# Optimization experiments

Hardware: AMD Instinct MI355X
Metric: run time of the kernel (lower is better)

The kernel has to match this reference:

```python
import jax, jax.numpy as jnp
import numpy as np

L, N, D = 2, 100000, 128
TRACE_HID, MVC_DIM, MVC_HID = 256, 128, 64
NUM_EDGE = 1600000
TAU = 0.5


def setup_inputs() -> dict:
    key = jax.random.key(0)
    ks = jax.random.split(key, 9)
    trace_all = jax.random.normal(ks[0], (L, N, D), dtype=jnp.float32)
    W_lin = jax.random.normal(ks[1], (TRACE_HID, L * D), dtype=jnp.float32) * 0.05
    W_lin2 = jax.random.normal(ks[2], (MVC_DIM, TRACE_HID), dtype=jnp.float32) * 0.05
    W_fc1 = jax.random.normal(ks[3], (MVC_HID, 2 * MVC_DIM), dtype=jnp.float32) * 0.05
    b_fc1 = jax.random.normal(ks[4], (MVC_HID,), dtype=jnp.float32) * 0.05
    W_fc2 = jax.random.normal(ks[5], (2, MVC_HID), dtype=jnp.float32) * 0.05
    b_fc2 = jax.random.normal(ks[6], (2,), dtype=jnp.float32) * 0.05
    u = jax.random.uniform(ks[7], (NUM_EDGE, 2), dtype=jnp.float32, minval=1e-6, maxval=1.0 - 1e-6)
    gumbel = -jnp.log(-jnp.log(u))  # standard Gumbel(0,1) noise
    edge_index = jax.random.randint(ks[8], (2, 3 * NUM_EDGE), 0, N, dtype=jnp.int32)
    return {
        "trace_all": trace_all, "W_lin": W_lin, "W_lin2": W_lin2,
        "W_fc1": W_fc1, "b_fc1": b_fc1, "W_fc2": W_fc2, "b_fc2": b_fc2,
        "gumbel": gumbel, "edge_index": edge_index, "num_edge": NUM_EDGE,
    }


def reference(trace_all, W_lin, W_lin2, W_fc1, b_fc1, W_fc2, b_fc2, gumbel, edge_index, num_edge):
    # --- TraceMLP: [L, N, d] -> mvc [N, mvc_dim] (eval mode: dropout is identity)
    l, n, d = trace_all.shape
    x = jnp.transpose(trace_all, (1, 0, 2)).reshape(n, l * d)      # [N, L*d]
    h = jax.nn.relu(x @ W_lin.T)                                   # [N, trace_hidden]
    mvc = h @ W_lin2.T                                             # [N, mvc_dim]
    norm = jnp.maximum(jnp.linalg.norm(mvc, axis=1, keepdims=True), 1e-12)
    mvc = mvc / norm                                               # F.normalize(p=2, dim=1)

    # --- EdgeScoringNet over non-slow edges (first num_edge columns)
    src = edge_index[0, :num_edge]
    dst = edge_index[1, :num_edge]
    comb = jnp.concatenate([mvc[src], mvc[dst]], axis=1)           # [E, 2*mvc_dim]
    h2 = jax.nn.relu(comb @ W_fc1.T + b_fc1)                       # [E, mvc_hidden]
    scores = h2 @ W_fc2.T + b_fc2                                  # [E, 2]

    # --- gumbel_softmax(tau=0.5, hard=True)[:, 0] (straight-through)
    y_soft = jax.nn.softmax((scores + gumbel) / TAU, axis=-1)
    y_hard = jax.nn.one_hot(jnp.argmax(y_soft, axis=-1), 2, dtype=y_soft.dtype)
    ret = y_hard - jax.lax.stop_gradient(y_soft) + y_soft
    active = ret[:, 0]                                             # [E], values in {0,1}

    # --- train_mask: first block = active, next two blocks = 1 - active
    train_mask = jnp.concatenate([active, 1.0 - active, 1.0 - active])  # [3*E]
    return train_mask
```

## Files before the change

### kernel.cpp

```cpp
#include <hip/hip_runtime.h>

#define NN   100000
#define EE   1600000
#define EROW 4800000

typedef _Float16 half8 __attribute__((ext_vector_type(8)));
typedef _Float16 half4 __attribute__((ext_vector_type(4)));
typedef float    f32x4 __attribute__((ext_vector_type(4)));

__device__ __forceinline__ float4 ld4(const float* p){ return *(const float4*)p; }

__device__ __forceinline__ unsigned splitf(float v) {
    _Float16 h = (_Float16)v;
    float r = v - (float)h;
    _Float16 l = (_Float16)(r * 2048.0f);
    union { _Float16 f; unsigned short u; } uh, ul;
    uh.f = h; ul.f = l;
    return (unsigned)uh.u | ((unsigned)ul.u << 16);
}

__device__ __forceinline__ void dma16(const void* g, void* l) {
    __builtin_amdgcn_global_load_lds(
        (const __attribute__((address_space(1))) unsigned*)((size_t)g),
        (__attribute__((address_space(3))) unsigned*)((size_t)l),
        16, 0, 0);
}

__global__ __launch_bounds__(256)
void prep_w(const float* __restrict__ W1, const float* __restrict__ W2,
            const float* __restrict__ W3, unsigned* __restrict__ o1,
            unsigned* __restrict__ o2, unsigned* __restrict__ o3)
{
    int idx = blockIdx.x * 256 + threadIdx.x;
    if (idx < 65536) {
        o1[idx] = splitf(W1[idx]);
    } else if (idx < 98304) {
        int i = idx - 65536;
        o2[i] = splitf(W2[i]);
    } else {
        int i = idx - 98304;
        int j = i >> 7, k = i & 127;
        o3[i] = splitf(W3[(j & 63) * 256 + (j >> 6) * 128 + k]);
    }
}

template<int SRCA, int EPI, int K>
__global__ __launch_bounds__(256, 2)
void gemm_mfma(const void* __restrict__ Asrc, const unsigned* __restrict__ Bw,
               const float* __restrict__ bias, unsigned* __restrict__ outS,
               float* __restrict__ outF, unsigned short* __restrict__ outH,
               int M, int No)
{
    __shared__ __align__(16) unsigned bufA[2][128 * 32];
    __shared__ __align__(16) unsigned bufB[2][128 * 32];
    __shared__ float sqv[128][2];

    const int t     = threadIdx.x;
    const int w     = t >> 6;
    const int wm    = w >> 1;
    const int wn    = w & 1;
    const int lane  = t & 63;
    const int lm    = lane & 15;
    const int q     = lane >> 4;
    const int mBase = blockIdx.x * 128;
    const int nBase = blockIdx.y * 128;

    const int col16 = (lane & 7) ^ (lane >> 3);

    f32x4 aH[4][4], aM[4][4];
#pragma unroll
    for (int i = 0; i < 4; ++i)
#pragma unroll
        for (int j = 0; j < 4; ++j) {
            aH[i][j] = (f32x4){0.f, 0.f, 0.f, 0.f};
            aM[i][j] = (f32x4){0.f, 0.f, 0.f, 0.f};
        }

    auto stage = [&](int sb, int kt) {
#pragma unroll
        for (int c = 0; c < 4; ++c) {
            const int row = w * 32 + c * 8 + (lane >> 3);
            unsigned* ldsA = &bufA[sb][w * 1024 + c * 256];
            unsigned* ldsB = &bufB[sb][w * 1024 + c * 256];
            int rgA = mBase + row; rgA = rgA < M ? rgA : M - 1;
            if (SRCA == 0) {
                const int kg    = kt * 32;
                const int plane = kg >> 7;
                const int ktl   = kg & 127;
                const float* gA = (const float*)Asrc
                    + (size_t)plane * ((size_t)NN * 128)
                    + (size_t)rgA * 128 + ktl + col16 * 4;
                dma16(gA, ldsA);
            } else {
                const unsigned* gA = (const unsigned*)Asrc
                    + (size_t)rgA * K + kt * 32 + col16 * 4;
                dma16(gA, ldsA);
            }
            const unsigned* gB = Bw + (size_t)(nBase + row) * K + kt * 32 + col16 * 4;
            dma16(gB, ldsB);
        }
    };

    union HL { uint4 u; half8 h; };

    constexpr int NK = K / 32;
    stage(0, 0);
    __syncthreads();

#pragma unroll 2
    for (int kt = 0; kt < NK; ++kt) {
        const int b = kt & 1;
        if (kt + 1 < NK) stage(b ^ 1, kt + 1);

        half8 fAh[4], fAl[4], fBh[4], fBl[4];

#pragma unroll
        for (int i = 0; i < 4; ++i) {
            const int r = wm * 64 + i * 16 + lm;
            const int x = r & 7;
            const unsigned* p0p = &bufA[b][r * 32 + (((2 * q) ^ x) << 2)];
            const unsigned* p1p = &bufA[b][r * 32 + ((((2 * q) | 1) ^ x) << 2)];
            HL H, L;
            if (SRCA == 0) {
                float4 f0 = *(const float4*)p0p;
                float4 f1 = *(const float4*)p1p;
                unsigned p0 = splitf(f0.x), p1 = splitf(f0.y);
                unsigned p2 = splitf(f0.z), p3 = splitf(f0.w);
                unsigned p4 = splitf(f1.x), p5 = splitf(f1.y);
                unsigned p6 = splitf(f1.z), p7 = splitf(f1.w);
                H.u.x = (p0 & 0xffffu) | (p1 << 16);
                H.u.y = (p2 & 0xffffu) | (p3 << 16);
                H.u.z = (p4 & 0xffffu) | (p5 << 16);
                H.u.w = (p6 & 0xffffu) | (p7 << 16);
                L.u.x = (p0 >> 16) | (p1 & 0xffff0000u);
                L.u.y = (p2 >> 16) | (p3 & 0xffff0000u);
                L.u.z = (p4 >> 16) | (p5 & 0xffff0000u);
                L.u.w = (p6 >> 16) | (p7 & 0xffff0000u);
            } else {
                uint4 u0 = *(const uint4*)p0p;
                uint4 u1 = *(const uint4*)p1p;
                H.u.x = (u0.x & 0xffffu) | (u0.y << 16);
                H.u.y = (u0.z & 0xffffu) | (u0.w << 16);
                H.u.z = (u1.x & 0xffffu) | (u1.y << 16);
                H.u.w = (u1.z & 0xffffu) | (u1.w << 16);
                L.u.x = (u0.x >> 16) | (u0.y & 0xffff0000u);
                L.u.y = (u0.z >> 16) | (u0.w & 0xffff0000u);
                L.u.z = (u1.x >> 16) | (u1.y & 0xffff0000u);
                L.u.w = (u1.z >> 16) | (u1.w & 0xffff0000u);
            }
            fAh[i] = H.h;
            fAl[i] = L.h;
        }

#pragma unroll
        for (int j = 0; j < 4; ++j) {
            const int r = wn * 64 + j * 16 + lm;
            const int x = r & 7;
            uint4 u0 = *(const uint4*)&bufB[b][r * 32 + (((2 * q) ^ x) << 2)];
            uint4 u1 = *(const uint4*)&bufB[b][r * 32 + ((((2 * q) | 1) ^ x) << 2)];
            HL H, L;
            H.u.x = (u0.x & 0xffffu) | (u0.y << 16);
            H.u.y = (u0.z & 0xffffu) | (u0.w << 16);
            H.u.z = (u1.x & 0xffffu) | (u1.y << 16);
            H.u.w = (u1.z & 0xffffu) | (u1.w << 16);
            L.u.x = (u0.x >> 16) | (u0.y & 0xffff0000u);
            L.u.y = (u0.z >> 16) | (u0.w & 0xffff0000u);
            L.u.z = (u1.x >> 16) | (u1.y & 0xffff0000u);
            L.u.w = (u1.z >> 16) | (u1.w & 0xffff0000u);
            fBh[j] = H.h;
            fBl[j] = L.h;
        }

        __builtin_amdgcn_s_setprio(1);
#pragma unroll
        for (int i = 0; i < 4; ++i)
#pragma unroll
            for (int j = 0; j < 4; ++j)
                aH[i][j] = __builtin_amdgcn_mfma_f32_16x16x32_f16(fAh[i], fBh[j], aH[i][j], 0, 0, 0);
#pragma unroll
        for (int i = 0; i < 4; ++i)
#pragma unroll
            for (int j = 0; j < 4; ++j)
                aM[i][j] = __builtin_amdgcn_mfma_f32_16x16x32_f16(fAh[i], fBl[j], aM[i][j], 0, 0, 0);
#pragma unroll
        for (int i = 0; i < 4; ++i)
#pragma unroll
            for (int j = 0; j < 4; ++j)
                aM[i][j] = __builtin_amdgcn_mfma_f32_16x16x32_f16(fAl[i], fBh[j], aM[i][j], 0, 0, 0);
        __builtin_amdgcn_s_setprio(0);

        if (kt + 1 < NK) __syncthreads();
    }

    const float cM = 1.0f / 2048.0f;
#pragma unroll
    for (int i = 0; i < 4; ++i)
#pragma unroll
        for (int j = 0; j < 4; ++j)
            aH[i][j] = aH[i][j] + aM[i][j] * cM;

    float nm[4][4];
    if (EPI == 1) {
#pragma unroll
        for (int i = 0; i < 4; ++i)
#pragma unroll
            for (int r = 0; r < 4; ++r) {
                float s = 0.f;
#pragma unroll
                for (int j = 0; j < 4; ++j) { float x = aH[i][j][r]; s = fmaf(x, x, s); }
#pragma unroll
                for (int off = 1; off < 16; off <<= 1) s += __shfl_xor(s, off, 16);
                if (lm == 0) sqv[wm * 64 + i * 16 + q * 4 + r][wn] = s;
            }
        __syncthreads();
#pragma unroll
        for (int i = 0; i < 4; ++i)
#pragma unroll
            for (int r = 0; r < 4; ++r) {
                const int rl = wm * 64 + i * 16 + q * 4 + r;
                nm[i][r] = fmaxf(sqrtf(sqv[rl][0] + sqv[rl][1]), 1e-12f);
            }
    }

    float bj[4] = {0.f, 0.f, 0.f, 0.f};
    if (EPI == 2 && wn == 0) {
#pragma unroll
        for (int j = 0; j < 4; ++j) bj[j] = bias[j * 16 + lm];
    }

#pragma unroll
    for (int i = 0; i < 4; ++i)
#pragma unroll
        for (int r = 0; r < 4; ++r) {
            const int m = mBase + wm * 64 + i * 16 + q * 4 + r;
            if (m < M) {
#pragma unroll
                for (int j = 0; j < 4; ++j) {
                    const int c = nBase + wn * 64 + j * 16 + lm;
                    float v = aH[i][j][r];
                    if (EPI == 0) { v = fmaxf(v, 0.f); outS[(size_t)m * No + c] = splitf(v); }
                    if (EPI == 1) { v = v / nm[i][r];  outS[(size_t)m * No + c] = splitf(v); }
                    if (EPI == 2) {
                        v += bj[j];
                        outF[(size_t)m * No + c] = v;
                        union { _Float16 f; unsigned short u; } cv; cv.f = (_Float16)v;
                        outH[(size_t)m * No + c] = cv.u;
                    }
                }
            }
        }
}

#define EPB 128
__global__ __launch_bounds__(256, 4)
void edge_k(const unsigned short* __restrict__ pH, const float* __restrict__ p,
            const int* __restrict__ ei, const float* __restrict__ gum,
            const float* __restrict__ W2, const float* __restrict__ b2,
            float* __restrict__ out)
{
    __shared__ int   sidx[EPB];
    __shared__ int   didx[EPB];
    __shared__ float gl[2 * EPB];
    __shared__ float act[EPB];

    const int t  = threadIdx.x;
    const int e0 = blockIdx.x * EPB;

    if (t < EPB) sidx[t] = ei[e0 + t];
    else         didx[t - EPB] = ei[EROW + e0 + (t - EPB)];
    gl[t] = gum[(size_t)e0 * 2 + t];
    __syncthreads();

    const int j   = t & 15;
    const int grp = t >> 4;
    const float4 w0 = ld4(&W2[j * 4]);
    const float4 w1 = ld4(&W2[64 + j * 4]);
    const float4 dk = make_float4(w0.x - w1.x, w0.y - w1.y,
                                  w0.z - w1.z, w0.w - w1.w);
    const float4 dw = make_float4(fabsf(dk.x), fabsf(dk.y),
                                  fabsf(dk.z), fabsf(dk.w));
    const float b20 = b2[0], b21 = b2[1];
    const float dB  = b20 - b21;

    union U8 { uint2 u; half4 h; };
    U8 ua[8], ub[8];
#pragma unroll
    for (int it = 0; it < 8; ++it) {
        const int el = grp * 8 + it;
        ua[it].u = *(const uint2*)&pH[(size_t)sidx[el] * 128 + j * 4];
        ub[it].u = *(const uint2*)&pH[(size_t)didx[el] * 128 + 64 + j * 4];
    }

#pragma unroll
    for (int it = 0; it < 8; ++it) {
        const int el = grp * 8 + it;
        const float a0 = (float)ua[it].h[0], a1 = (float)ua[it].h[1];
        const float a2 = (float)ua[it].h[2], a3 = (float)ua[it].h[3];
        const float c0 = (float)ub[it].h[0], c1 = (float)ub[it].h[1];
        const float c2 = (float)ub[it].h[2], c3 = (float)ub[it].h[3];
        const float r0 = fmaxf(a0 + c0, 0.f);
        const float r1 = fmaxf(a1 + c1, 0.f);
        const float r2 = fmaxf(a2 + c2, 0.f);
        const float r3 = fmaxf(a3 + c3, 0.f);
        float sc = r0 * dk.x + r1 * dk.y + r2 * dk.z + r3 * dk.w;
        float eb = dw.x * (fabsf(a0) + fabsf(c0)) + dw.y * (fabsf(a1) + fabsf(c1))
                 + dw.z * (fabsf(a2) + fabsf(c2)) + dw.w * (fabsf(a3) + fabsf(c3));
#pragma unroll
        for (int off = 1; off < 16; off <<= 1) {
            sc += __shfl_xor(sc, off, 16);
            eb += __shfl_xor(eb, off, 16);
        }
        const float g0 = gl[el * 2], g1 = gl[el * 2 + 1];
        const float gap = sc + dB + (g0 - g1);
        const float bound = eb * 0.0009765625f + 2e-5f;
        float av;
        if (fabsf(gap) > bound) {
            av = (gap >= 0.f) ? 1.f : 0.f;
        } else {
            const float4 pa = ld4(&p[(size_t)sidx[el] * 128 + j * 4]);
            const float4 pb = ld4(&p[(size_t)didx[el] * 128 + 64 + j * 4]);
            const float q0 = fmaxf(pa.x + pb.x, 0.f);
            const float q1 = fmaxf(pa.y + pb.y, 0.f);
            const float q2 = fmaxf(pa.z + pb.z, 0.f);
            const float q3 = fmaxf(pa.w + pb.w, 0.f);
            float t0 = q0 * w0.x + q1 * w0.y + q2 * w0.z + q3 * w0.w;
            float t1 = q0 * w1.x + q1 * w1.y + q2 * w1.z + q3 * w1.w;
#pragma unroll
            for (int off = 1; off < 16; off <<= 1) {
                t0 += __shfl_xor(t0, off, 16);
                t1 += __shfl_xor(t1, off, 16);
            }
            const float ge = (t0 + b20 + g0) - (t1 + b21 + g1);
            av = (ge >= 0.f) ? 1.f : 0.f;
        }
        if (j == 0) act[el] = av;
    }
    __syncthreads();

    if (t < EPB) {
        const float a = act[t];
        const size_t e = (size_t)e0 + t;
        out[e]                  = a;
        out[EE + e]             = 1.f - a;
        out[2 * (size_t)EE + e] = 1.f - a;
    }
}

extern "C" void kernel_launch(void* const* d_in, const int* in_sizes, int n_in,
                              void* d_out, int out_size, void* d_ws, size_t ws_size,
                              hipStream_t stream)
{
    const float* trace  = (const float*)d_in[0];
    const float* W_lin  = (const float*)d_in[1];
    const float* W_lin2 = (const float*)d_in[2];
    const float* W_fc1  = (const float*)d_in[3];
    const float* b_fc1  = (const float*)d_in[4];
    const float* W_fc2  = (const float*)d_in[5];
    const float* b_fc2  = (const float*)d_in[6];
    const float* gum    = (const float*)d_in[7];
    const int*   ei     = (const int*)  d_in[8];
    float*       out    = (float*)d_out;

    char* ws = (char*)d_ws;
    unsigned*       hpl = (unsigned*)ws;
    unsigned*       mpl = (unsigned*)(ws + (size_t)NN * 256 * 4);
    unsigned*       W1i = (unsigned*)(ws + (size_t)NN * 256 * 4 + (size_t)NN * 128 * 4);
    unsigned*       W2i = W1i + 65536;
    unsigned*       W3i = W2i + 32768;
    float*          p   = (float*)ws;
    unsigned short* pH  = (unsigned short*)(ws + (size_t)NN * 128 * 4);

    prep_w<<<448, 256, 0, stream>>>(W_lin, W_lin2, W_fc1, W1i, W2i, W3i);

    const int mB = (NN + 127) / 128;

    gemm_mfma<0, 0, 256><<<dim3(mB, 2), 256, 0, stream>>>(trace, W1i, nullptr, hpl, nullptr, nullptr, NN, 256);
    gemm_mfma<1, 1, 256><<<dim3(mB, 1), 256, 0, stream>>>(hpl, W2i, nullptr, mpl, nullptr, nullptr, NN, 128);
    gemm_mfma<1, 2, 128><<<dim3(mB, 1), 256, 0, stream>>>(mpl, W3i, b_fc1, nullptr, p, pH, NN, 128);
    edge_k<<<EE / EPB, 256, 0, stream>>>(pH, p, ei, gum, W_fc2, b_fc2, out);
}
```

Before: 369.9 us.

## Shrink GEMM tile to 128x64 and defer L2 normalization into the third GEMM

The MFMA GEMM tile drops from 128x128 to 128x64 with all four waves split along M. Each kernel launches twice as many blocks, and the launch bound rises to 3 blocks per CU for higher occupancy. The row L2 normalization moves out of the second GEMM's epilogue. The third GEMM now computes the row sum of squares from its A-operand fragments and divides its outputs by the norm, which is valid because normalization is a row scale that commutes with the linear layer. The cost is more redundant A-tile loads across N blocks and extra ALU work per fragment in the third GEMM.

```diff
diff --git a/kernel.cpp b/kernel.cpp
--- a/kernel.cpp
+++ b/kernel.cpp
@@ -45,57 +45,59 @@
 }
 
 template<int SRCA, int EPI, int K>
-__global__ __launch_bounds__(256, 2)
+__global__ __launch_bounds__(256, 3)
 void gemm_mfma(const void* __restrict__ Asrc, const unsigned* __restrict__ Bw,
                const float* __restrict__ bias, unsigned* __restrict__ outS,
                float* __restrict__ outF, unsigned short* __restrict__ outH,
                int M, int No)
 {
     __shared__ __align__(16) unsigned bufA[2][128 * 32];
-    __shared__ __align__(16) unsigned bufB[2][128 * 32];
-    __shared__ float sqv[128][2];
+    __shared__ __align__(16) unsigned bufB[2][64 * 32];
+    __shared__ float sqv[128];
 
     const int t     = threadIdx.x;
     const int w     = t >> 6;
-    const int wm    = w >> 1;
-    const int wn    = w & 1;
     const int lane  = t & 63;
     const int lm    = lane & 15;
     const int q     = lane >> 4;
     const int mBase = blockIdx.x * 128;
-    const int nBase = blockIdx.y * 128;
+    const int nBase = blockIdx.y * 64;
 
     const int col16 = (lane & 7) ^ (lane >> 3);
 
-    f32x4 aH[4][4], aM[4][4];
-#pragma unroll
-    for (int i = 0; i < 4; ++i)
+    f32x4 aH[2][4], aM[2][4];
+#pragma unroll
+    for (int i = 0; i < 2; ++i)
 #pragma unroll
         for (int j = 0; j < 4; ++j) {
             aH[i][j] = (f32x4){0.f, 0.f, 0.f, 0.f};
             aM[i][j] = (f32x4){0.f, 0.f, 0.f, 0.f};
         }
 
+    float ssq[2] = {0.f, 0.f};
+
     auto stage = [&](int sb, int kt) {
 #pragma unroll
         for (int c = 0; c < 4; ++c) {
             const int row = w * 32 + c * 8 + (lane >> 3);
             unsigned* ldsA = &bufA[sb][w * 1024 + c * 256];
-            unsigned* ldsB = &bufB[sb][w * 1024 + c * 256];
             int rgA = mBase + row; rgA = rgA < M ? rgA : M - 1;
             if (SRCA == 0) {
-                const int kg    = kt * 32;
-                const int plane = kg >> 7;
-                const int ktl   = kg & 127;
+                const int kg = kt * 32;
                 const float* gA = (const float*)Asrc
-                    + (size_t)plane * ((size_t)NN * 128)
-                    + (size_t)rgA * 128 + ktl + col16 * 4;
+                    + (size_t)(kg >> 7) * ((size_t)NN * 128)
+                    + (size_t)rgA * 128 + (kg & 127) + col16 * 4;
                 dma16(gA, ldsA);
             } else {
                 const unsigned* gA = (const unsigned*)Asrc
                     + (size_t)rgA * K + kt * 32 + col16 * 4;
                 dma16(gA, ldsA);
             }
+        }
+#pragma unroll
+        for (int c = 0; c < 2; ++c) {
+            const int row = w * 16 + c * 8 + (lane >> 3);
+            unsigned* ldsB = &bufB[sb][w * 512 + c * 256];
             const unsigned* gB = Bw + (size_t)(nBase + row) * K + kt * 32 + col16 * 4;
             dma16(gB, ldsB);
         }
@@ -112,12 +114,11 @@
         const int b = kt & 1;
         if (kt + 1 < NK) stage(b ^ 1, kt + 1);
 
-        half8 fAh[4], fAl[4], fBh[4], fBl[4];
-
-#pragma unroll
-        for (int i = 0; i < 4; ++i) {
-            const int r = wm * 64 + i * 16 + lm;
-            const int x = r & 7;
+        half8 fAh[2], fAl[2];
+#pragma unroll
+        for (int i = 0; i < 2; ++i) {
+            const int r = w * 32 + i * 16 + lm;
+            const int x = lm & 7;
             const unsigned* p0p = &bufA[b][r * 32 + (((2 * q) ^ x) << 2)];
             const unsigned* p1p = &bufA[b][r * 32 + ((((2 * q) | 1) ^ x) << 2)];
             HL H, L;
@@ -150,14 +151,22 @@
             }
             fAh[i] = H.h;
             fAl[i] = L.h;
-        }
-
+            if (EPI == 2) {
+#pragma unroll
+                for (int e = 0; e < 8; ++e) {
+                    float v = (float)fAh[i][e] + (float)fAl[i][e] * (1.0f / 2048.0f);
+                    ssq[i] = fmaf(v, v, ssq[i]);
+                }
+            }
+        }
+
+        __builtin_amdgcn_s_setprio(1);
 #pragma unroll
         for (int j = 0; j < 4; ++j) {
-            const int r = wn * 64 + j * 16 + lm;
-            const int x = r & 7;
-            uint4 u0 = *(const uint4*)&bufB[b][r * 32 + (((2 * q) ^ x) << 2)];
-            uint4 u1 = *(const uint4*)&bufB[b][r * 32 + ((((2 * q) | 1) ^ x) << 2)];
+            const int rB = j * 16 + lm;
+            const int x = lm & 7;
+            uint4 u0 = *(const uint4*)&bufB[b][rB * 32 + (((2 * q) ^ x) << 2)];
+            uint4 u1 = *(const uint4*)&bufB[b][rB * 32 + ((((2 * q) | 1) ^ x) << 2)];
             HL H, L;
             H.u.x = (u0.x & 0xffffu) | (u0.y << 16);
             H.u.y = (u0.z & 0xffffu) | (u0.w << 16);
@@ -167,26 +176,13 @@
             L.u.y = (u0.z >> 16) | (u0.w & 0xffff0000u);
             L.u.z = (u1.x >> 16) | (u1.y & 0xffff0000u);
             L.u.w = (u1.z >> 16) | (u1.w & 0xffff0000u);
-            fBh[j] = H.h;
-            fBl[j] = L.h;
-        }
-
-        __builtin_amdgcn_s_setprio(1);
-#pragma unroll
-        for (int i = 0; i < 4; ++i)
-#pragma unroll
-            for (int j = 0; j < 4; ++j)
-                aH[i][j] = __builtin_amdgcn_mfma_f32_16x16x32_f16(fAh[i], fBh[j], aH[i][j], 0, 0, 0);
-#pragma unroll
-        for (int i = 0; i < 4; ++i)
-#pragma unroll
-            for (int j = 0; j < 4; ++j)
-                aM[i][j] = __builtin_amdgcn_mfma_f32_16x16x32_f16(fAh[i], fBl[j], aM[i][j], 0, 0, 0);
-#pragma unroll
-        for (int i = 0; i < 4; ++i)
-#pragma unroll
-            for (int j = 0; j < 4; ++j)
-                aM[i][j] = __builtin_amdgcn_mfma_f32_16x16x32_f16(fAl[i], fBh[j], aM[i][j], 0, 0, 0);
+#pragma unroll
+            for (int i = 0; i < 2; ++i) {
+                aH[i][j] = __builtin_amdgcn_mfma_f32_16x16x32_f16(fAh[i], H.h, aH[i][j], 0, 0, 0);
+                aM[i][j] = __builtin_amdgcn_mfma_f32_16x16x32_f16(fAh[i], L.h, aM[i][j], 0, 0, 0);
+                aM[i][j] = __builtin_amdgcn_mfma_f32_16x16x32_f16(fAl[i], H.h, aM[i][j], 0, 0, 0);
+            }
+        }
         __builtin_amdgcn_s_setprio(0);
 
         if (kt + 1 < NK) __syncthreads();
@@ -194,54 +190,45 @@
 
     const float cM = 1.0f / 2048.0f;
 #pragma unroll
-    for (int i = 0; i < 4; ++i)
+    for (int i = 0; i < 2; ++i)
 #pragma unroll
         for (int j = 0; j < 4; ++j)
             aH[i][j] = aH[i][j] + aM[i][j] * cM;
 
-    float nm[4][4];
-    if (EPI == 1) {
-#pragma unroll
-        for (int i = 0; i < 4; ++i)
-#pragma unroll
-            for (int r = 0; r < 4; ++r) {
-                float s = 0.f;
-#pragma unroll
-                for (int j = 0; j < 4; ++j) { float x = aH[i][j][r]; s = fmaf(x, x, s); }
-#pragma unroll
-                for (int off = 1; off < 16; off <<= 1) s += __shfl_xor(s, off, 16);
-                if (lm == 0) sqv[wm * 64 + i * 16 + q * 4 + r][wn] = s;
-            }
+    if (EPI == 2) {
+#pragma unroll
+        for (int i = 0; i < 2; ++i) {
+            float s = ssq[i];
+            s += __shfl_xor(s, 16);
+            s += __shfl_xor(s, 32);
+            if (q == 0) sqv[w * 32 + i * 16 + lm] = s;
+        }
         __syncthreads();
-#pragma unroll
-        for (int i = 0; i < 4; ++i)
-#pragma unroll
-            for (int r = 0; r < 4; ++r) {
-                const int rl = wm * 64 + i * 16 + q * 4 + r;
-                nm[i][r] = fmaxf(sqrtf(sqv[rl][0] + sqv[rl][1]), 1e-12f);
-            }
     }
 
     float bj[4] = {0.f, 0.f, 0.f, 0.f};
-    if (EPI == 2 && wn == 0) {
+    if (EPI == 2 && nBase == 0 && bias) {
 #pragma unroll
         for (int j = 0; j < 4; ++j) bj[j] = bias[j * 16 + lm];
     }
 
 #pragma unroll
-    for (int i = 0; i < 4; ++i)
+    for (int i = 0; i < 2; ++i)
 #pragma unroll
         for (int r = 0; r < 4; ++r) {
-            const int m = mBase + wm * 64 + i * 16 + q * 4 + r;
+            const int m = mBase + w * 32 + i * 16 + q * 4 + r;
             if (m < M) {
+                float nm = 1.f;
+                if (EPI == 2)
+                    nm = fmaxf(sqrtf(sqv[w * 32 + i * 16 + q * 4 + r]), 1e-12f);
 #pragma unroll
                 for (int j = 0; j < 4; ++j) {
-                    const int c = nBase + wn * 64 + j * 16 + lm;
+                    const int c = nBase + j * 16 + lm;
                     float v = aH[i][j][r];
                     if (EPI == 0) { v = fmaxf(v, 0.f); outS[(size_t)m * No + c] = splitf(v); }
-                    if (EPI == 1) { v = v / nm[i][r];  outS[(size_t)m * No + c] = splitf(v); }
+                    if (EPI == 1) { outS[(size_t)m * No + c] = splitf(v); }
                     if (EPI == 2) {
-                        v += bj[j];
+                        v = v / nm + bj[j];
                         outF[(size_t)m * No + c] = v;
                         union { _Float16 f; unsigned short u; } cv; cv.f = (_Float16)v;
                         outH[(size_t)m * No + c] = cv.u;
@@ -374,8 +361,8 @@
 
     const int mB = (NN + 127) / 128;
 
-    gemm_mfma<0, 0, 256><<<dim3(mB, 2), 256, 0, stream>>>(trace, W1i, nullptr, hpl, nullptr, nullptr, NN, 256);
-    gemm_mfma<1, 1, 256><<<dim3(mB, 1), 256, 0, stream>>>(hpl, W2i, nullptr, mpl, nullptr, nullptr, NN, 128);
-    gemm_mfma<1, 2, 128><<<dim3(mB, 1), 256, 0, stream>>>(mpl, W3i, b_fc1, nullptr, p, pH, NN, 128);
+    gemm_mfma<0, 0, 256><<<dim3(mB, 4), 256, 0, stream>>>(trace, W1i, nullptr, hpl, nullptr, nullptr, NN, 256);
+    gemm_mfma<1, 1, 256><<<dim3(mB, 2), 256, 0, stream>>>(hpl, W2i, nullptr, mpl, nullptr, nullptr, NN, 128);
+    gemm_mfma<1, 2, 128><<<dim3(mB, 2), 256, 0, stream>>>(mpl, W3i, b_fc1, nullptr, p, pH, NN, 128);
     edge_k<<<EE / EPB, 256, 0, stream>>>(pH, p, ei, gum, W_fc2, b_fc2, out);
 }
```

Result: slower. 390.8 us (+5.6%).

## Fuse second and third GEMMs and store projection as fp16 hi/lo halves

Applied to the files above, without the earlier changes.

Merges the normalize GEMM and the fc1 projection GEMM into one kernel. The normalized mvc tile stays in LDS as split-fp16 pairs and is immediately multiplied by W_fc1, which removes the mvc round trip through global memory and one launch. The fp32 projection buffer is replaced by a separate fp16 low-residual array. The edge kernel's fallback path rebuilds near-fp32 values from the high halves it already loaded plus the low halves. The cost is reading W3 fragments directly from global memory inside the fused kernel, plus extra LDS pressure.

```diff
diff --git a/kernel.cpp b/kernel.cpp
--- a/kernel.cpp
+++ b/kernel.cpp
@@ -44,16 +44,13 @@
     }
 }
 
-template<int SRCA, int EPI, int K>
+template<int SRCA, int K>
 __global__ __launch_bounds__(256, 2)
 void gemm_mfma(const void* __restrict__ Asrc, const unsigned* __restrict__ Bw,
-               const float* __restrict__ bias, unsigned* __restrict__ outS,
-               float* __restrict__ outF, unsigned short* __restrict__ outH,
-               int M, int No)
+               unsigned* __restrict__ outS, int M, int No)
 {
     __shared__ __align__(16) unsigned bufA[2][128 * 32];
     __shared__ __align__(16) unsigned bufB[2][128 * 32];
-    __shared__ float sqv[128][2];
 
     const int t     = threadIdx.x;
     const int w     = t >> 6;
@@ -84,12 +81,10 @@
             unsigned* ldsB = &bufB[sb][w * 1024 + c * 256];
             int rgA = mBase + row; rgA = rgA < M ? rgA : M - 1;
             if (SRCA == 0) {
-                const int kg    = kt * 32;
-                const int plane = kg >> 7;
-                const int ktl   = kg & 127;
+                const int kg = kt * 32;
                 const float* gA = (const float*)Asrc
-                    + (size_t)plane * ((size_t)NN * 128)
-                    + (size_t)rgA * 128 + ktl + col16 * 4;
+                    + (size_t)(kg >> 7) * ((size_t)NN * 128)
+                    + (size_t)rgA * 128 + (kg & 127) + col16 * 4;
                 dma16(gA, ldsA);
             } else {
                 const unsigned* gA = (const unsigned*)Asrc
@@ -199,35 +194,6 @@
         for (int j = 0; j < 4; ++j)
             aH[i][j] = aH[i][j] + aM[i][j] * cM;
 
-    float nm[4][4];
-    if (EPI == 1) {
-#pragma unroll
-        for (int i = 0; i < 4; ++i)
-#pragma unroll
-            for (int r = 0; r < 4; ++r) {
-                float s = 0.f;
-#pragma unroll
-                for (int j = 0; j < 4; ++j) { float x = aH[i][j][r]; s = fmaf(x, x, s); }
-#pragma unroll
-                for (int off = 1; off < 16; off <<= 1) s += __shfl_xor(s, off, 16);
-                if (lm == 0) sqv[wm * 64 + i * 16 + q * 4 + r][wn] = s;
-            }
-        __syncthreads();
-#pragma unroll
-        for (int i = 0; i < 4; ++i)
-#pragma unroll
-            for (int r = 0; r < 4; ++r) {
-                const int rl = wm * 64 + i * 16 + q * 4 + r;
-                nm[i][r] = fmaxf(sqrtf(sqv[rl][0] + sqv[rl][1]), 1e-12f);
-            }
-    }
-
-    float bj[4] = {0.f, 0.f, 0.f, 0.f};
-    if (EPI == 2 && wn == 0) {
-#pragma unroll
-        for (int j = 0; j < 4; ++j) bj[j] = bias[j * 16 + lm];
-    }
-
 #pragma unroll
     for (int i = 0; i < 4; ++i)
 #pragma unroll
@@ -237,23 +203,237 @@
 #pragma unroll
                 for (int j = 0; j < 4; ++j) {
                     const int c = nBase + wn * 64 + j * 16 + lm;
-                    float v = aH[i][j][r];
-                    if (EPI == 0) { v = fmaxf(v, 0.f); outS[(size_t)m * No + c] = splitf(v); }
-                    if (EPI == 1) { v = v / nm[i][r];  outS[(size_t)m * No + c] = splitf(v); }
-                    if (EPI == 2) {
-                        v += bj[j];
-                        outF[(size_t)m * No + c] = v;
-                        union { _Float16 f; unsigned short u; } cv; cv.f = (_Float16)v;
-                        outH[(size_t)m * No + c] = cv.u;
-                    }
+                    float v = fmaxf(aH[i][j][r], 0.f);
+                    outS[(size_t)m * No + c] = splitf(v);
                 }
             }
         }
 }
 
+__global__ __launch_bounds__(256, 2)
+void gemm23(const unsigned* __restrict__ Apl, const unsigned* __restrict__ W2i,
+            const unsigned* __restrict__ W3i, const float* __restrict__ bias,
+            unsigned short* __restrict__ pHo, unsigned short* __restrict__ pLo,
+            int M)
+{
+    __shared__ __align__(16) unsigned smem[16384];
+    __shared__ float sqv[128][2];
+    unsigned (*bufA)[128 * 32] = (unsigned(*)[128 * 32])(smem);
+    unsigned (*bufB)[128 * 32] = (unsigned(*)[128 * 32])(smem + 8192);
+    unsigned* mld = smem;
+
+    const int t     = threadIdx.x;
+    const int w     = t >> 6;
+    const int wm    = w >> 1;
+    const int wn    = w & 1;
+    const int lane  = t & 63;
+    const int lm    = lane & 15;
+    const int q     = lane >> 4;
+    const int mBase = blockIdx.x * 128;
+
+    const int col16 = (lane & 7) ^ (lane >> 3);
+    const float cM = 1.0f / 2048.0f;
+
+    f32x4 aH[4][4], aM[4][4];
+#pragma unroll
+    for (int i = 0; i < 4; ++i)
+#pragma unroll
+        for (int j = 0; j < 4; ++j) {
+            aH[i][j] = (f32x4){0.f, 0.f, 0.f, 0.f};
+            aM[i][j] = (f32x4){0.f, 0.f, 0.f, 0.f};
+        }
+
+    auto stage = [&](int sb, int kt) {
+#pragma unroll
+        for (int c = 0; c < 4; ++c) {
+            const int row = w * 32 + c * 8 + (lane >> 3);
+            unsigned* ldsA = &bufA[sb][w * 1024 + c * 256];
+            unsigned* ldsB = &bufB[sb][w * 1024 + c * 256];
+            int rgA = mBase + row; rgA = rgA < M ? rgA : M - 1;
+            const unsigned* gA = Apl + (size_t)rgA * 256 + kt * 32 + col16 * 4;
+            dma16(gA, ldsA);
+            const unsigned* gB = W2i + (size_t)row * 256 + kt * 32 + col16 * 4;
+            dma16(gB, ldsB);
+        }
+    };
+
+    union HL { uint4 u; half8 h; };
+
+    auto deint = [&](uint4 u0, uint4 u1, half8& hh, half8& hl) {
+        HL H, L;
+        H.u.x = (u0.x & 0xffffu) | (u0.y << 16);
+        H.u.y = (u0.z & 0xffffu) | (u0.w << 16);
+        H.u.z = (u1.x & 0xffffu) | (u1.y << 16);
+        H.u.w = (u1.z & 0xffffu) | (u1.w << 16);
+        L.u.x = (u0.x >> 16) | (u0.y & 0xffff0000u);
+        L.u.y = (u0.z >> 16) | (u0.w & 0xffff0000u);
+        L.u.z = (u1.x >> 16) | (u1.y & 0xffff0000u);
+        L.u.w = (u1.z >> 16) | (u1.w & 0xffff0000u);
+        hh = H.h; hl = L.h;
+    };
+
+    stage(0, 0);
+    __syncthreads();
+
+#pragma unroll 2
+    for (int kt = 0; kt < 8; ++kt) {
+        const int b = kt & 1;
+        if (kt + 1 < 8) stage(b ^ 1, kt + 1);
+
+        half8 fAh[4], fAl[4], fBh[4], fBl[4];
+#pragma unroll
+        for (int i = 0; i < 4; ++i) {
+            const int r = wm * 64 + i * 16 + lm;
+            const int x = r & 7;
+            uint4 u0 = *(const uint4*)&bufA[b][r * 32 + (((2 * q) ^ x) << 2)];
+            uint4 u1 = *(const uint4*)&bufA[b][r * 32 + ((((2 * q) | 1) ^ x) << 2)];
+            deint(u0, u1, fAh[i], fAl[i]);
+        }
+#pragma unroll
+        for (int j = 0; j < 4; ++j) {
+            const int r = wn * 64 + j * 16 + lm;
+            const int x = r & 7;
+            uint4 u0 = *(const uint4*)&bufB[b][r * 32 + (((2 * q) ^ x) << 2)];
+            uint4 u1 = *(const uint4*)&bufB[b][r * 32 + ((((2 * q) | 1) ^ x) << 2)];
+            deint(u0, u1, fBh[j], fBl[j]);
+        }
+
+        __builtin_amdgcn_s_setprio(1);
+#pragma unroll
+        for (int i = 0; i < 4; ++i)
+#pragma unroll
+            for (int j = 0; j < 4; ++j)
+                aH[i][j] = __builtin_amdgcn_mfma_f32_16x16x32_f16(fAh[i], fBh[j], aH[i][j], 0, 0, 0);
+#pragma unroll
+        for (int i = 0; i < 4; ++i)
+#pragma unroll
+            for (int j = 0; j < 4; ++j)
+                aM[i][j] = __builtin_amdgcn_mfma_f32_16x16x32_f16(fAh[i], fBl[j], aM[i][j], 0, 0, 0);
+#pragma unroll
+        for (int i = 0; i < 4; ++i)
+#pragma unroll
+            for (int j = 0; j < 4; ++j)
+                aM[i][j] = __builtin_amdgcn_mfma_f32_16x16x32_f16(fAl[i], fBh[j], aM[i][j], 0, 0, 0);
+        __builtin_amdgcn_s_setprio(0);
+
+        if (kt + 1 < 8) __syncthreads();
+    }
+
+#pragma unroll
+    for (int i = 0; i < 4; ++i)
+#pragma unroll
+        for (int j = 0; j < 4; ++j)
+            aH[i][j] = aH[i][j] + aM[i][j] * cM;
+
+#pragma unroll
+    for (int i = 0; i < 4; ++i)
+#pragma unroll
+        for (int r = 0; r < 4; ++r) {
+            float s = 0.f;
+#pragma unroll
+            for (int j = 0; j < 4; ++j) { float x = aH[i][j][r]; s = fmaf(x, x, s); }
+#pragma unroll
+            for (int off = 1; off < 16; off <<= 1) s += __shfl_xor(s, off, 16);
+            if (lm == 0) sqv[wm * 64 + i * 16 + q * 4 + r][wn] = s;
+        }
+    __syncthreads();
+
+#pragma unroll
+    for (int i = 0; i < 4; ++i)
+#pragma unroll
+        for (int r = 0; r < 4; ++r) {
+            const int rl = wm * 64 + i * 16 + q * 4 + r;
+            const float nm = fmaxf(sqrtf(sqv[rl][0] + sqv[rl][1]), 1e-12f);
+#pragma unroll
+            for (int j = 0; j < 4; ++j) {
+                const int col = wn * 64 + j * 16 + lm;
+                const int ch  = (col >> 2) ^ (rl & 15);
+                mld[rl * 128 + (ch << 2) + (col & 3)] = splitf(aH[i][j][r] / nm);
+            }
+        }
+    __syncthreads();
+
+#pragma unroll
+    for (int i = 0; i < 4; ++i)
+#pragma unroll
+        for (int j = 0; j < 4; ++j) {
+            aH[i][j] = (f32x4){0.f, 0.f, 0.f, 0.f};
+            aM[i][j] = (f32x4){0.f, 0.f, 0.f, 0.f};
+        }
+
+#pragma unroll
+    for (int kt = 0; kt < 4; ++kt) {
+        half8 fAh[4], fAl[4], fBh[4], fBl[4];
+#pragma unroll
+        for (int i = 0; i < 4; ++i) {
+            const int row = wm * 64 + i * 16 + lm;
+            const int x = row & 15;
+            const int c0 = kt * 8 + 2 * q;
+            uint4 u0 = *(const uint4*)&mld[row * 128 + ((c0 ^ x) << 2)];
+            uint4 u1 = *(const uint4*)&mld[row * 128 + (((c0 + 1) ^ x) << 2)];
+            deint(u0, u1, fAh[i], fAl[i]);
+        }
+#pragma unroll
+        for (int j = 0; j < 4; ++j) {
+            const int row = wn * 64 + j * 16 + lm;
+            const unsigned* bp = W3i + (size_t)row * 128 + kt * 32 + q * 8;
+            uint4 u0 = *(const uint4*)bp;
+            uint4 u1 = *(const uint4*)(bp + 4);
+            deint(u0, u1, fBh[j], fBl[j]);
+        }
+
+        __builtin_amdgcn_s_setprio(1);
+#pragma unroll
+        for (int i = 0; i < 4; ++i)
+#pragma unroll
+            for (int j = 0; j < 4; ++j)
+                aH[i][j] = __builtin_amdgcn_mfma_f32_16x16x32_f16(fAh[i], fBh[j], aH[i][j], 0, 0, 0);
+#pragma unroll
+        for (int i = 0; i < 4; ++i)
+#pragma unroll
+            for (int j = 0; j < 4; ++j)
+                aM[i][j] = __builtin_amdgcn_mfma_f32_16x16x32_f16(fAh[i], fBl[j], aM[i][j], 0, 0, 0);
+#pragma unroll
+        for (int i = 0; i < 4; ++i)
+#pragma unroll
+            for (int j = 0; j < 4; ++j)
+                aM[i][j] = __builtin_amdgcn_mfma_f32_16x16x32_f16(fAl[i], fBh[j], aM[i][j], 0, 0, 0);
+        __builtin_amdgcn_s_setprio(0);
+    }
+
+#pragma unroll
+    for (int i = 0; i < 4; ++i)
+#pragma unroll
+        for (int j = 0; j < 4; ++j)
+            aH[i][j] = aH[i][j] + aM[i][j] * cM;
+
+    float bj[4] = {0.f, 0.f, 0.f, 0.f};
+    if (wn == 0) {
+#pragma unroll
+        for (int j = 0; j < 4; ++j) bj[j] = bias[j * 16 + lm];
+    }
+
+#pragma unroll
+    for (int i = 0; i < 4; ++i)
+#pragma unroll
+        for (int r = 0; r < 4; ++r) {
+            const int m = mBase + wm * 64 + i * 16 + q * 4 + r;
+            if (m < M) {
+#pragma unroll
+                for (int j = 0; j < 4; ++j) {
+                    const int c = wn * 64 + j * 16 + lm;
+                    const float v = aH[i][j][r] + bj[j];
+                    const unsigned pk = splitf(v);
+                    pHo[(size_t)m * 128 + c] = (unsigned short)(pk & 0xffffu);
+                    pLo[(size_t)m * 128 + c] = (unsigned short)(pk >> 16);
+                }
+            }
+        }
+}
+
 #define EPB 128
 __global__ __launch_bounds__(256, 4)
-void edge_k(const unsigned short* __restrict__ pH, const float* __restrict__ p,
+void edge_k(const unsigned short* __restrict__ pH, const unsigned short* __restrict__ pL,
             const int* __restrict__ ei, const float* __restrict__ gum,
             const float* __restrict__ W2, const float* __restrict__ b2,
             float* __restrict__ out)
@@ -317,12 +497,14 @@
         if (fabsf(gap) > bound) {
             av = (gap >= 0.f) ? 1.f : 0.f;
         } else {
-            const float4 pa = ld4(&p[(size_t)sidx[el] * 128 + j * 4]);
-            const float4 pb = ld4(&p[(size_t)didx[el] * 128 + 64 + j * 4]);
-            const float q0 = fmaxf(pa.x + pb.x, 0.f);
-            const float q1 = fmaxf(pa.y + pb.y, 0.f);
-            const float q2 = fmaxf(pa.z + pb.z, 0.f);
-            const float q3 = fmaxf(pa.w + pb.w, 0.f);
+            U8 la, lb;
+            la.u = *(const uint2*)&pL[(size_t)sidx[el] * 128 + j * 4];
+            lb.u = *(const uint2*)&pL[(size_t)didx[el] * 128 + 64 + j * 4];
+            const float iS = 1.0f / 2048.0f;
+            const float q0 = fmaxf((a0 + (float)la.h[0] * iS) + (c0 + (float)lb.h[0] * iS), 0.f);
+            const float q1 = fmaxf((a1 + (float)la.h[1] * iS) + (c1 + (float)lb.h[1] * iS), 0.f);
+            const float q2 = fmaxf((a2 + (float)la.h[2] * iS) + (c2 + (float)lb.h[2] * iS), 0.f);
+            const float q3 = fmaxf((a3 + (float)la.h[3] * iS) + (c3 + (float)lb.h[3] * iS), 0.f);
             float t0 = q0 * w0.x + q1 * w0.y + q2 * w0.z + q3 * w0.w;
             float t1 = q0 * w1.x + q1 * w1.y + q2 * w1.z + q3 * w1.w;
 #pragma unroll
@@ -363,19 +545,17 @@
 
     char* ws = (char*)d_ws;
     unsigned*       hpl = (unsigned*)ws;
-    unsigned*       mpl = (unsigned*)(ws + (size_t)NN * 256 * 4);
+    unsigned short* pH  = (unsigned short*)(ws + (size_t)NN * 256 * 4);
+    unsigned short* pL  = (unsigned short*)(ws + (size_t)NN * 256 * 4 + (size_t)NN * 128 * 2);
     unsigned*       W1i = (unsigned*)(ws + (size_t)NN * 256 * 4 + (size_t)NN * 128 * 4);
     unsigned*       W2i = W1i + 65536;
     unsigned*       W3i = W2i + 32768;
-    float*          p   = (float*)ws;
-    unsigned short* pH  = (unsigned short*)(ws + (size_t)NN * 128 * 4);
 
     prep_w<<<448, 256, 0, stream>>>(W_lin, W_lin2, W_fc1, W1i, W2i, W3i);
 
     const int mB = (NN + 127) / 128;
 
-    gemm_mfma<0, 0, 256><<<dim3(mB, 2), 256, 0, stream>>>(trace, W1i, nullptr, hpl, nullptr, nullptr, NN, 256);
-    gemm_mfma<1, 1, 256><<<dim3(mB, 1), 256, 0, stream>>>(hpl, W2i, nullptr, mpl, nullptr, nullptr, NN, 128);
-    gemm_mfma<1, 2, 128><<<dim3(mB, 1), 256, 0, stream>>>(mpl, W3i, b_fc1, nullptr, p, pH, NN, 128);
-    edge_k<<<EE / EPB, 256, 0, stream>>>(pH, p, ei, gum, W_fc2, b_fc2, out);
-}
+    gemm_mfma<0, 256><<<dim3(mB, 2), 256, 0, stream>>>(trace, W1i, hpl, NN, 256);
+    gemm23<<<mB, 256, 0, stream>>>(hpl, W2i, W3i, b_fc1, pH, pL, NN);
+    edge_k<<<EE / EPB, 256, 0, stream>>>(pH, pL, ei, gum, W_fc2, b_fc2, out);
+}
```

Result: faster. 358.5 us, median of 2 (-3.1%).
